# Kernel optimization log

Measured on AMD Instinct MI355X. Metric: run time of the kernel, lower is better.

## Reference

```python
import jax, jax.numpy as jnp
import numpy as np

EPS = 1e-06
NUM_HEADS = 16
THETA = 10000.0


def rope_tables(grid_size, head_dim):
    # matches VisionRotaryEmbeddingFast: 2D rope, table shape [grid^2, head_dim]
    half = head_dim // 2
    freqs = 1.0 / THETA ** (jnp.arange(0, half, 2, dtype=jnp.float32) / half)
    freqs = jnp.concatenate([freqs, freqs], axis=0)  # [half]
    t = jnp.arange(grid_size, dtype=jnp.float32)
    f = jnp.outer(t, freqs)  # [grid, half]
    fh = jnp.broadcast_to(f[:, None, :], (grid_size, grid_size, half))
    fw = jnp.broadcast_to(f[None, :, :], (grid_size, grid_size, half))
    full = jnp.concatenate([fh, fw], axis=-1).reshape(-1, head_dim)  # [N, head_dim]
    return jnp.cos(full), jnp.sin(full)


def rotate_half(x):
    n = x.shape[-1] // 2
    return jnp.concatenate((-x[..., n:], x[..., :n]), axis=-1)


def rms_norm(x, gamma):
    var = jnp.mean(x * x, axis=-1, keepdims=True)
    return x * jax.lax.rsqrt(var + EPS) * gamma


def setup_inputs() -> dict:
    key = jax.random.key(0)
    ks = jax.random.split(key, 5)
    B, N, C = 32, 1024, 1024
    return {
        "x": jax.random.normal(ks[0], (B, N, C), dtype=jnp.float32),
        "qkv_w": jax.random.normal(ks[1], (C, 3 * C), dtype=jnp.float32) * (C ** -0.5),
        "qkv_b": jnp.zeros((3 * C,), dtype=jnp.float32),
        "proj_w": jax.random.normal(ks[2], (C, C), dtype=jnp.float32) * (C ** -0.5),
        "proj_b": jnp.zeros((C,), dtype=jnp.float32),
        "q_gamma": jnp.ones((C // NUM_HEADS,), dtype=jnp.float32),
        "k_gamma": jnp.ones((C // NUM_HEADS,), dtype=jnp.float32),
    }


def reference(x, qkv_w, qkv_b, proj_w, proj_b, q_gamma, k_gamma):
    B, N, C = x.shape
    H = NUM_HEADS
    hd = C // H
    grid = int(np.sqrt(N))
    cos, sin = rope_tables(grid, hd)  # [N, hd] each
    cos = cos[None, :, None, :]  # broadcast over [B, N, H, hd]
    sin = sin[None, :, None, :]

    qkv = (x @ qkv_w + qkv_b).reshape(B, N, 3, H, hd)
    q, k, v = qkv[:, :, 0], qkv[:, :, 1], qkv[:, :, 2]  # [B, N, H, hd]

    q = rms_norm(q, q_gamma)
    k = rms_norm(k, k_gamma)
    q = q * cos + rotate_half(q) * sin
    k = k * cos + rotate_half(k) * sin

    out = jax.nn.dot_product_attention(q, k, v, is_causal=False)  # [B, N, H, hd]
    out = out.reshape(B, N, C)
    return out @ proj_w + proj_b
```

## Files before the change

kernel.cpp:

```cpp
#include <hip/hip_runtime.h>
#include <stdint.h>

typedef float f32x4 __attribute__((ext_vector_type(4)));
typedef short s16x8 __attribute__((ext_vector_type(8)));
typedef unsigned short u16;

__device__ __forceinline__ u16 f2bf(float f) {
  union { float f; uint32_t u; } c; c.f = f;
  uint32_t u = c.u;
  u = (u + 0x7fffu + ((u >> 16) & 1u)) >> 16;
  return (u16)u;
}

__device__ __forceinline__ u16 f2bf_fast(float f) {
  union { float f; uint32_t u; } c; c.f = f;
  return (u16)((c.u + 0x8000u) >> 16);
}

__device__ __forceinline__ void gload16(const void* g, void* lds) {
  __builtin_amdgcn_global_load_lds(
      (const __attribute__((address_space(1))) void*)g,
      (__attribute__((address_space(3))) void*)lds, 16, 0, 0);
}

__device__ __forceinline__ f32x4 mfma16(s16x8 a, s16x8 b, f32x4 c) {
  return __builtin_amdgcn_mfma_f32_16x16x32_bf16(a, b, c, 0, 0, 0);
}

__device__ __forceinline__ int swz(int row, int c8) {
  return row * 64 + ((c8 ^ (row & 7)) << 3);
}

__global__ void cvt_bf16(const float* __restrict__ in, u16* __restrict__ out, size_t n) {
  size_t i = ((size_t)blockIdx.x * blockDim.x + threadIdx.x) * 4;
  if (i < n) {
    float4 v = *(const float4*)&in[i];
    u16 o0 = f2bf(v.x), o1 = f2bf(v.y), o2 = f2bf(v.z), o3 = f2bf(v.w);
    uint2 packed;
    packed.x = (uint32_t)o0 | ((uint32_t)o1 << 16);
    packed.y = (uint32_t)o2 | ((uint32_t)o3 << 16);
    *(uint2*)&out[i] = packed;
  }
}

__global__ void transpose_cvt(const float* __restrict__ in, u16* __restrict__ out,
                              int rows, int cols) {
  __shared__ float tile[64][65];
  const int c0 = blockIdx.x * 64, r0 = blockIdx.y * 64;
  const int tr = threadIdx.x >> 6, tc = threadIdx.x & 63;
#pragma unroll
  for (int i = 0; i < 16; i++) {
    int r = i * 4 + tr;
    tile[r][tc] = in[(size_t)(r0 + r) * cols + c0 + tc];
  }
  __syncthreads();
#pragma unroll
  for (int i = 0; i < 16; i++) {
    int oc = i * 4 + tr;
    out[(size_t)(c0 + oc) * rows + r0 + tc] = f2bf(tile[tc][oc]);
  }
}

__global__ void rope_tables_kernel(float* __restrict__ cosT, float* __restrict__ sinT) {
  int n = blockIdx.x;
  int d = threadIdx.x;
  int ph = n >> 5, pw = n & 31;
  int pos = (d < 32) ? ph : pw;
  int fi = d & 15;
  float freq = powf(10000.f, -(float)fi / 16.f);
  float ang = (float)pos * freq;
  cosT[n * 64 + d] = cosf(ang);
  sinT[n * 64 + d] = sinf(ang);
}

__device__ __forceinline__ void gemm_mainloop_1024(
    const u16* __restrict__ Ag, const u16* __restrict__ Bg,
    u16* As, u16* Bs, f32x4 (&acc)[4][4])
{
  const int t = threadIdx.x;
  const int l = t & 63, w = t >> 6;
  const int wm = w >> 1, wn = w & 1;
  const int lrow = l & 15, lk8 = (l >> 4) * 8;
  const int row0 = t >> 2, cc = (t & 3) * 8;

  for (int kt = 0; kt < 1024; kt += 32) {
    gload16(Ag + (size_t)row0 * 1024 + kt + cc,        &As[w * 512]);
    gload16(Ag + (size_t)(row0 + 64) * 1024 + kt + cc, &As[2048 + w * 512]);
    gload16(Bg + (size_t)row0 * 1024 + kt + cc,        &Bs[w * 512]);
    gload16(Bg + (size_t)(row0 + 64) * 1024 + kt + cc, &Bs[2048 + w * 512]);
    asm volatile("s_waitcnt vmcnt(0)" ::: "memory");
    __syncthreads();

    s16x8 af[4], bfr[4];
#pragma unroll
    for (int mt = 0; mt < 4; mt++)
      af[mt] = *(const s16x8*)&As[(wm * 64 + mt * 16 + lrow) * 32 + lk8];
#pragma unroll
    for (int nt = 0; nt < 4; nt++)
      bfr[nt] = *(const s16x8*)&Bs[(wn * 64 + nt * 16 + lrow) * 32 + lk8];
#pragma unroll
    for (int mt = 0; mt < 4; mt++)
#pragma unroll
      for (int nt = 0; nt < 4; nt++)
        acc[mt][nt] = mfma16(af[mt], bfr[nt], acc[mt][nt]);
    __syncthreads();
  }
}

__global__ __launch_bounds__(256, 2) void gemm_qkv(
    const u16* __restrict__ A,
    const u16* __restrict__ Bt,
    const float* __restrict__ bias,
    const float* __restrict__ qgam, const float* __restrict__ kgam,
    const float* __restrict__ cosT, const float* __restrict__ sinT,
    u16* __restrict__ qb, u16* __restrict__ kb, u16* __restrict__ vb)
{
  __shared__ u16 As[4096], Bs[4096];
  const int bn = blockIdx.x, bm = blockIdx.y;

  const f32x4 fzero = {0.f, 0.f, 0.f, 0.f};
  f32x4 acc[4][4];
#pragma unroll
  for (int i = 0; i < 4; i++)
#pragma unroll
    for (int j = 0; j < 4; j++) acc[i][j] = fzero;

  gemm_mainloop_1024(A + (size_t)bm * 128 * 1024, Bt + (size_t)bn * 128 * 1024, As, Bs, acc);

  const int t = threadIdx.x, l = t & 63, w = t >> 6;
  const int wm = w >> 1, wn = w & 1, lrow = l & 15, lg = l >> 4;
  const int colb = bn * 128 + wn * 64;
  const int s = colb >> 10;
  const int h = (colb & 1023) >> 6;

  float biasv[4], g[4];
#pragma unroll
  for (int nt = 0; nt < 4; nt++) biasv[nt] = bias[colb + nt * 16 + lrow];
  const float* gamma = (s == 0) ? qgam : kgam;
#pragma unroll
  for (int nt = 0; nt < 4; nt++) g[nt] = gamma[nt * 16 + lrow];

  if (s < 2) {
    u16* dst = (s == 0) ? qb : kb;
    const float mul = (s == 0) ? 0.18033688011112042f : 1.0f;
#pragma unroll
    for (int mt = 0; mt < 4; mt++) {
#pragma unroll
      for (int r = 0; r < 4; r++) {
        const int rowg = bm * 128 + wm * 64 + mt * 16 + lg * 4 + r;
        const int b = rowg >> 10, np = rowg & 1023;
        float tmp[4]; float sq = 0.f;
#pragma unroll
        for (int nt = 0; nt < 4; nt++) {
          float v = acc[mt][nt][r] + biasv[nt];
          tmp[nt] = v; sq += v * v;
        }
#pragma unroll
        for (int off = 1; off < 16; off <<= 1) sq += __shfl_xor(sq, off);
        const float rstd = rsqrtf(sq * 0.015625f + 1e-6f);
#pragma unroll
        for (int nt = 0; nt < 4; nt++) tmp[nt] *= rstd * g[nt];
        const size_t base = (((size_t)(b * 16 + h)) * 1024 + np) * 64;
#pragma unroll
        for (int nt = 0; nt < 4; nt++) {
          const int d = nt * 16 + lrow;
          const float cv = cosT[np * 64 + d], sv = sinT[np * 64 + d];
          const float rh = (nt < 2) ? -tmp[nt + 2] : tmp[nt - 2];
          dst[base + d] = f2bf((tmp[nt] * cv + rh * sv) * mul);
        }
      }
    }
  } else {
#pragma unroll
    for (int mt = 0; mt < 4; mt++) {
#pragma unroll
      for (int r = 0; r < 4; r++) {
        const int rowg = bm * 128 + wm * 64 + mt * 16 + lg * 4 + r;
        const int b = rowg >> 10, np = rowg & 1023;
        const size_t hb = ((size_t)(b * 16 + h)) * 64;
#pragma unroll
        for (int nt = 0; nt < 4; nt++) {
          const int d = nt * 16 + lrow;
          vb[(hb + d) * 1024 + np] = f2bf(acc[mt][nt][r] + biasv[nt]);
        }
      }
    }
  }
}

__global__ __launch_bounds__(256, 3) void attn_kernel(
    const u16* __restrict__ qbuf, const u16* __restrict__ kbuf,
    const u16* __restrict__ vtbuf, u16* __restrict__ obuf)
{
  __shared__ u16 Qs[128 * 64];
  __shared__ u16 Ks[64 * 64];
  __shared__ u16 VTs[64 * 64];
  __shared__ u16 Ps[128 * 64];
  const int bx = blockIdx.x;
  const int bh = bx >> 3, qt = bx & 7;
  const int t = threadIdx.x, l = t & 63, w = t >> 6;
  const int lrow = l & 15, lg = l >> 4;

  const u16* qg  = qbuf  + (size_t)bh * 65536 + (size_t)qt * 8192;
  const u16* kg0 = kbuf  + (size_t)bh * 65536;
  const u16* vt0 = vtbuf + (size_t)bh * 65536;

  const int srow = l >> 3;
  const int sc8  = (l & 7) ^ (srow & 7);

#pragma unroll
  for (int i = 0; i < 4; i++) {
    const int r0 = (w + i * 4) * 8;
    gload16(qg + (size_t)(r0 + srow) * 64 + sc8 * 8, &Qs[r0 * 64]);
  }
#pragma unroll
  for (int i = 0; i < 2; i++) {
    const int r0 = (w + i * 4) * 8;
    gload16(kg0 + (size_t)(r0 + srow) * 64 + sc8 * 8, &Ks[r0 * 64]);
    gload16(vt0 + (size_t)(r0 + srow) * 1024 + sc8 * 8, &VTs[r0 * 64]);
  }
  asm volatile("s_waitcnt vmcnt(0)" ::: "memory");
  __syncthreads();

  s16x8 aq[2][2];
#pragma unroll
  for (int mt = 0; mt < 2; mt++)
#pragma unroll
    for (int kh = 0; kh < 2; kh++)
      aq[mt][kh] = *(const s16x8*)&Qs[swz(w * 32 + mt * 16 + lrow, kh * 4 + lg)];

  const f32x4 fzero = {0.f, 0.f, 0.f, 0.f};
  f32x4 o[2][4];
  float l_[2][4];
#pragma unroll
  for (int mt = 0; mt < 2; mt++) {
#pragma unroll
    for (int dt = 0; dt < 4; dt++) o[mt][dt] = fzero;
#pragma unroll
    for (int r = 0; r < 4; r++) l_[mt][r] = 0.f;
  }

  for (int kt = 0; kt < 16; kt++) {
    s16x8 bk[4][2];
#pragma unroll
    for (int nt = 0; nt < 4; nt++)
#pragma unroll
      for (int kh = 0; kh < 2; kh++)
        bk[nt][kh] = *(const s16x8*)&Ks[swz(nt * 16 + lrow, kh * 4 + lg)];

    f32x4 sf[2][4];
#pragma unroll
    for (int mt = 0; mt < 2; mt++)
#pragma unroll
      for (int nt = 0; nt < 4; nt++) {
        f32x4 z = fzero;
        z = mfma16(aq[mt][0], bk[nt][0], z);
        z = mfma16(aq[mt][1], bk[nt][1], z);
        sf[mt][nt] = z;
      }

#pragma unroll
    for (int mt = 0; mt < 2; mt++) {
      const int rowb = w * 32 + mt * 16 + lg * 4;
#pragma unroll
      for (int r = 0; r < 4; r++) {
        const int row = rowb + r;
        u16* prow = &Ps[row * 64 + (lrow & 7)];
        const int rm = row & 7;
        float acc_l = 0.f;
#pragma unroll
        for (int nt = 0; nt < 4; nt++) {
          float p = __builtin_amdgcn_exp2f(sf[mt][nt][r]);
          acc_l += p;
          prow[((nt * 2 + (lrow >> 3)) ^ rm) << 3] = f2bf_fast(p);
        }
        l_[mt][r] += acc_l;
      }
    }
    asm volatile("s_waitcnt lgkmcnt(0)" ::: "memory");

    s16x8 ap[2][2], bv[4][2];
#pragma unroll
    for (int mt = 0; mt < 2; mt++)
#pragma unroll
      for (int kh = 0; kh < 2; kh++)
        ap[mt][kh] = *(const s16x8*)&Ps[swz(w * 32 + mt * 16 + lrow, kh * 4 + lg)];
#pragma unroll
    for (int dt = 0; dt < 4; dt++)
#pragma unroll
      for (int kh = 0; kh < 2; kh++)
        bv[dt][kh] = *(const s16x8*)&VTs[swz(dt * 16 + lrow, kh * 4 + lg)];
#pragma unroll
    for (int mt = 0; mt < 2; mt++)
#pragma unroll
      for (int dt = 0; dt < 4; dt++) {
        o[mt][dt] = mfma16(ap[mt][0], bv[dt][0], o[mt][dt]);
        o[mt][dt] = mfma16(ap[mt][1], bv[dt][1], o[mt][dt]);
      }

    __syncthreads();
    if (kt < 15) {
      const int kb = (kt + 1) * 64;
#pragma unroll
      for (int i = 0; i < 2; i++) {
        const int r0 = (w + i * 4) * 8;
        gload16(kg0 + (size_t)(kb + r0 + srow) * 64 + sc8 * 8, &Ks[r0 * 64]);
        gload16(vt0 + (size_t)(r0 + srow) * 1024 + kb + sc8 * 8, &VTs[r0 * 64]);
      }
      asm volatile("s_waitcnt vmcnt(0)" ::: "memory");
      __syncthreads();
    }
  }

  const int b = bh >> 4, h = bh & 15;
#pragma unroll
  for (int mt = 0; mt < 2; mt++)
#pragma unroll
    for (int r = 0; r < 4; r++) {
      float lsum = l_[mt][r];
#pragma unroll
      for (int off = 1; off < 16; off <<= 1) lsum += __shfl_xor(lsum, off);
      const float inv = 1.0f / lsum;
      const int n = qt * 128 + w * 32 + mt * 16 + lg * 4 + r;
      const size_t base = (((size_t)b * 1024 + n) * 16 + h) * 64;
#pragma unroll
      for (int dt = 0; dt < 4; dt++)
        obuf[base + dt * 16 + lrow] = f2bf(o[mt][dt][r] * inv);
    }
}

__global__ __launch_bounds__(256, 2) void gemm_proj(
    const u16* __restrict__ A,
    const u16* __restrict__ Bt,
    const float* __restrict__ bias,
    float* __restrict__ out)
{
  __shared__ u16 As[4096], Bs[4096];
  const int bn = blockIdx.x, bm = blockIdx.y;

  const f32x4 fzero = {0.f, 0.f, 0.f, 0.f};
  f32x4 acc[4][4];
#pragma unroll
  for (int i = 0; i < 4; i++)
#pragma unroll
    for (int j = 0; j < 4; j++) acc[i][j] = fzero;

  gemm_mainloop_1024(A + (size_t)bm * 128 * 1024, Bt + (size_t)bn * 128 * 1024, As, Bs, acc);

  const int t = threadIdx.x, l = t & 63, w = t >> 6;
  const int wm = w >> 1, wn = w & 1, lrow = l & 15, lg = l >> 4;
  float biasv[4];
#pragma unroll
  for (int nt = 0; nt < 4; nt++) biasv[nt] = bias[bn * 128 + wn * 64 + nt * 16 + lrow];

#pragma unroll
  for (int mt = 0; mt < 4; mt++) {
#pragma unroll
    for (int r = 0; r < 4; r++) {
      const int rowg = bm * 128 + wm * 64 + mt * 16 + lg * 4 + r;
#pragma unroll
      for (int nt = 0; nt < 4; nt++) {
        const int col = bn * 128 + wn * 64 + nt * 16 + lrow;
        out[(size_t)rowg * 1024 + col] = acc[mt][nt][r] + biasv[nt];
      }
    }
  }
}

extern "C" void kernel_launch(void* const* d_in, const int* in_sizes, int n_in,
                              void* d_out, int out_size, void* d_ws, size_t ws_size,
                              hipStream_t stream) {
  const float* x      = (const float*)d_in[0];
  const float* qkv_w  = (const float*)d_in[1];
  const float* qkv_b  = (const float*)d_in[2];
  const float* proj_w = (const float*)d_in[3];
  const float* proj_b = (const float*)d_in[4];
  const float* q_gam  = (const float*)d_in[5];
  const float* k_gam  = (const float*)d_in[6];

  char* ws = (char*)d_ws;
  u16*   xb   = (u16*)(ws);
  u16*   qb   = (u16*)(ws + 67108864);
  u16*   kb   = (u16*)(ws + 134217728);
  u16*   vb   = (u16*)(ws + 201326592);
  u16*   wqT  = (u16*)(ws + 268435456);
  u16*   wpT  = (u16*)(ws + 274726912);
  float* cosT = (float*)(ws + 276824064);
  float* sinT = (float*)(ws + 277086208);
  u16*   attn = xb;

  cvt_bf16<<<32768, 256, 0, stream>>>(x, xb, (size_t)33554432);
  transpose_cvt<<<dim3(48, 16), 256, 0, stream>>>(qkv_w, wqT, 1024, 3072);
  transpose_cvt<<<dim3(16, 16), 256, 0, stream>>>(proj_w, wpT, 1024, 1024);
  rope_tables_kernel<<<1024, 64, 0, stream>>>(cosT, sinT);

  gemm_qkv<<<dim3(24, 256), 256, 0, stream>>>(xb, wqT, qkv_b, q_gam, k_gam,
                                              cosT, sinT, qb, kb, vb);
  attn_kernel<<<4096, 256, 0, stream>>>(qb, kb, vb, attn);
  gemm_proj<<<dim3(8, 256), 256, 0, stream>>>(attn, wpT, proj_b, (float*)d_out);
}
```

Measured before the change: 795.5 us.

## Rewrite GEMM mainloop as 256x256 double-buffered 8-wave pipeline with swizzled LDS

Replaces the simple 128x128, k=32, fully-synchronous GEMM mainloop used by the QKV and projection GEMMs. The new loop uses 256x256 tiles, 8 waves and k=64 steps, double-buffers LDS and interleaves global->LDS prefetch with MFMA phases using s_setprio and barriers. It also adds XOR-swizzled LDS addressing and a block-index remap for L2 locality. The aim is to hide global load latency and raise data reuse, at the cost of 128KB of LDS per block, more accumulator registers and fragile hand-coded vmcnt accounting.

```diff
diff --git a/kernel.cpp b/kernel.cpp
--- a/kernel.cpp
+++ b/kernel.cpp
@@ -73,41 +73,110 @@
   sinT[n * 64 + d] = sinf(ang);
 }
 
-__device__ __forceinline__ void gemm_mainloop_1024(
+
+#define PH_MID \
+  __builtin_amdgcn_sched_barrier(0); \
+  __builtin_amdgcn_s_barrier(); \
+  asm volatile("s_waitcnt lgkmcnt(0)" ::: "memory"); \
+  __builtin_amdgcn_sched_barrier(0); \
+  __builtin_amdgcn_s_setprio(1);
+
+#define PH_END \
+  __builtin_amdgcn_s_setprio(0); \
+  __builtin_amdgcn_sched_barrier(0); \
+  __builtin_amdgcn_s_barrier(); \
+  __builtin_amdgcn_sched_barrier(0);
+
+#define STAGE(ldsoff, g) do { \
+    gload16((g) + (size_t)(w8 + srow) * 1024 + sc8 * 8,       &lds[(ldsoff) + w8 * 64]); \
+    gload16((g) + (size_t)(w8 + srow + 64) * 1024 + sc8 * 8,  &lds[(ldsoff) + (w8 + 64) * 64]); \
+  } while (0)
+
+#define RD_A(dst, BUF, mh) \
+  _Pragma("unroll") \
+  for (int mi = 0; mi < 4; mi++) { \
+    dst[mi][0] = *(const s16x8*)&lds[(BUF) * 32768 + arow0 + ((mh) * 64 + mi * 16) * 64 + swz0]; \
+    dst[mi][1] = *(const s16x8*)&lds[(BUF) * 32768 + arow0 + ((mh) * 64 + mi * 16) * 64 + swz1]; \
+  }
+
+#define RD_B(dst, BUF, nh) \
+  _Pragma("unroll") \
+  for (int ni = 0; ni < 2; ni++) { \
+    dst[ni][0] = *(const s16x8*)&lds[(BUF) * 32768 + 16384 + brow0 + ((nh) * 32 + ni * 16) * 64 + swz0]; \
+    dst[ni][1] = *(const s16x8*)&lds[(BUF) * 32768 + 16384 + brow0 + ((nh) * 32 + ni * 16) * 64 + swz1]; \
+  }
+
+#define MFMA_QUAD(af, bfr, mh, nh) \
+  _Pragma("unroll") \
+  for (int mi = 0; mi < 4; mi++) \
+    _Pragma("unroll") \
+    for (int ni = 0; ni < 2; ni++) { \
+      acc[(mh) * 4 + mi][(nh) * 2 + ni] = mfma16(af[mi][0], bfr[ni][0], acc[(mh) * 4 + mi][(nh) * 2 + ni]); \
+      acc[(mh) * 4 + mi][(nh) * 2 + ni] = mfma16(af[mi][1], bfr[ni][1], acc[(mh) * 4 + mi][(nh) * 2 + ni]); \
+    }
+
+#define KTILE(BUF, KT, MODE) do { \
+    s16x8 a0f[4][2], a1f[4][2], b0f[2][2], b1f[2][2]; \
+     \
+    RD_A(a0f, BUF, 0); \
+    RD_B(b0f, BUF, 0); \
+    if ((MODE) < 2) STAGE((1 - (BUF)) * 32768, Ag + (size_t)((KT) + 1) * 64); \
+    PH_MID; MFMA_QUAD(a0f, b0f, 0, 0); PH_END; \
+     \
+    RD_B(b1f, BUF, 1); \
+    if ((MODE) < 2) STAGE((1 - (BUF)) * 32768 + 8192, Ag + (size_t)128 * 1024 + ((KT) + 1) * 64); \
+    PH_MID; MFMA_QUAD(a0f, b1f, 0, 1); PH_END; \
+     \
+    RD_A(a1f, BUF, 1); \
+    if ((MODE) == 0) STAGE((BUF) * 32768 + 16384, Bg + (size_t)((KT) + 2) * 64); \
+    PH_MID; MFMA_QUAD(a1f, b1f, 1, 1); PH_END; \
+     \
+    if ((MODE) == 0) STAGE((BUF) * 32768 + 16384 + 8192, Bg + (size_t)128 * 1024 + ((KT) + 2) * 64); \
+    PH_MID; MFMA_QUAD(a1f, b0f, 1, 0); \
+    __builtin_amdgcn_s_setprio(0); \
+    if ((MODE) == 0) asm volatile("s_waitcnt vmcnt(4)" ::: "memory"); \
+    if ((MODE) == 1) asm volatile("s_waitcnt vmcnt(0)" ::: "memory"); \
+    __builtin_amdgcn_sched_barrier(0); \
+    __builtin_amdgcn_s_barrier(); \
+    __builtin_amdgcn_sched_barrier(0); \
+  } while (0)
+
+__device__ __forceinline__ void gemm_mainloop_8ph(
     const u16* __restrict__ Ag, const u16* __restrict__ Bg,
-    u16* As, u16* Bs, f32x4 (&acc)[4][4])
+    u16* lds, f32x4 (&acc)[8][4])
 {
   const int t = threadIdx.x;
   const int l = t & 63, w = t >> 6;
-  const int wm = w >> 1, wn = w & 1;
-  const int lrow = l & 15, lk8 = (l >> 4) * 8;
-  const int row0 = t >> 2, cc = (t & 3) * 8;
-
-  for (int kt = 0; kt < 1024; kt += 32) {
-    gload16(Ag + (size_t)row0 * 1024 + kt + cc,        &As[w * 512]);
-    gload16(Ag + (size_t)(row0 + 64) * 1024 + kt + cc, &As[2048 + w * 512]);
-    gload16(Bg + (size_t)row0 * 1024 + kt + cc,        &Bs[w * 512]);
-    gload16(Bg + (size_t)(row0 + 64) * 1024 + kt + cc, &Bs[2048 + w * 512]);
-    asm volatile("s_waitcnt vmcnt(0)" ::: "memory");
-    __syncthreads();
-
-    s16x8 af[4], bfr[4];
-#pragma unroll
-    for (int mt = 0; mt < 4; mt++)
-      af[mt] = *(const s16x8*)&As[(wm * 64 + mt * 16 + lrow) * 32 + lk8];
-#pragma unroll
-    for (int nt = 0; nt < 4; nt++)
-      bfr[nt] = *(const s16x8*)&Bs[(wn * 64 + nt * 16 + lrow) * 32 + lk8];
-#pragma unroll
-    for (int mt = 0; mt < 4; mt++)
-#pragma unroll
-      for (int nt = 0; nt < 4; nt++)
-        acc[mt][nt] = mfma16(af[mt], bfr[nt], acc[mt][nt]);
-    __syncthreads();
-  }
-}
-
-__global__ __launch_bounds__(256, 2) void gemm_qkv(
+  const int wm = w & 1, wn = w >> 1;
+  const int lrow = l & 15, lg = l >> 4;
+  const int srow = l >> 3, sc8 = (l & 7) ^ srow;
+  const int w8 = w * 8;
+  const int swz0 = ((0 + lg) ^ (lrow & 7)) << 3;
+  const int swz1 = ((4 + lg) ^ (lrow & 7)) << 3;
+  const int arow0 = (wm * 128 + lrow) * 64;
+  const int brow0 = (wn * 64 + lrow) * 64;
+
+  STAGE(0,                 Ag);
+  STAGE(8192,              Ag + (size_t)128 * 1024);
+  STAGE(16384,             Bg);
+  STAGE(16384 + 8192,      Bg + (size_t)128 * 1024);
+  STAGE(32768 + 16384,          Bg + 64);
+  STAGE(32768 + 16384 + 8192,   Bg + (size_t)128 * 1024 + 64);
+  asm volatile("s_waitcnt vmcnt(4)" ::: "memory");
+  __builtin_amdgcn_sched_barrier(0);
+  __builtin_amdgcn_s_barrier();
+  __builtin_amdgcn_sched_barrier(0);
+
+#pragma unroll 1
+  for (int kt = 0; kt < 14; kt += 2) {
+    KTILE(0, kt, 0);
+    KTILE(1, kt + 1, 0);
+  }
+  KTILE(0, 14, 1);
+  KTILE(1, 15, 2);
+}
+
+__global__ __launch_bounds__(512, 2) void gemm_qkv(
     const u16* __restrict__ A,
     const u16* __restrict__ Bt,
     const float* __restrict__ bias,
@@ -115,21 +184,23 @@
     const float* __restrict__ cosT, const float* __restrict__ sinT,
     u16* __restrict__ qb, u16* __restrict__ kb, u16* __restrict__ vb)
 {
-  __shared__ u16 As[4096], Bs[4096];
-  const int bn = blockIdx.x, bm = blockIdx.y;
+  __shared__ u16 lds[65536];
+  const int bid = blockIdx.x;
+  const int sb = (bid & 7) * 192 + (bid >> 3);
+  const int bm = sb / 12, bn = sb % 12;
 
   const f32x4 fzero = {0.f, 0.f, 0.f, 0.f};
-  f32x4 acc[4][4];
-#pragma unroll
-  for (int i = 0; i < 4; i++)
+  f32x4 acc[8][4];
+#pragma unroll
+  for (int i = 0; i < 8; i++)
 #pragma unroll
     for (int j = 0; j < 4; j++) acc[i][j] = fzero;
 
-  gemm_mainloop_1024(A + (size_t)bm * 128 * 1024, Bt + (size_t)bn * 128 * 1024, As, Bs, acc);
+  gemm_mainloop_8ph(A + (size_t)bm * 256 * 1024, Bt + (size_t)bn * 256 * 1024, lds, acc);
 
   const int t = threadIdx.x, l = t & 63, w = t >> 6;
-  const int wm = w >> 1, wn = w & 1, lrow = l & 15, lg = l >> 4;
-  const int colb = bn * 128 + wn * 64;
+  const int wm = w & 1, wn = w >> 1, lrow = l & 15, lg = l >> 4;
+  const int colb = bn * 256 + wn * 64;
   const int s = colb >> 10;
   const int h = (colb & 1023) >> 6;
 
@@ -144,15 +215,15 @@
     u16* dst = (s == 0) ? qb : kb;
     const float mul = (s == 0) ? 0.18033688011112042f : 1.0f;
 #pragma unroll
-    for (int mt = 0; mt < 4; mt++) {
+    for (int mf = 0; mf < 8; mf++) {
 #pragma unroll
       for (int r = 0; r < 4; r++) {
-        const int rowg = bm * 128 + wm * 64 + mt * 16 + lg * 4 + r;
+        const int rowg = bm * 256 + wm * 128 + mf * 16 + lg * 4 + r;
         const int b = rowg >> 10, np = rowg & 1023;
         float tmp[4]; float sq = 0.f;
 #pragma unroll
         for (int nt = 0; nt < 4; nt++) {
-          float v = acc[mt][nt][r] + biasv[nt];
+          float v = acc[mf][nt][r] + biasv[nt];
           tmp[nt] = v; sq += v * v;
         }
 #pragma unroll
@@ -172,16 +243,16 @@
     }
   } else {
 #pragma unroll
-    for (int mt = 0; mt < 4; mt++) {
+    for (int mf = 0; mf < 8; mf++) {
 #pragma unroll
       for (int r = 0; r < 4; r++) {
-        const int rowg = bm * 128 + wm * 64 + mt * 16 + lg * 4 + r;
+        const int rowg = bm * 256 + wm * 128 + mf * 16 + lg * 4 + r;
         const int b = rowg >> 10, np = rowg & 1023;
         const size_t hb = ((size_t)(b * 16 + h)) * 64;
 #pragma unroll
         for (int nt = 0; nt < 4; nt++) {
           const int d = nt * 16 + lrow;
-          vb[(hb + d) * 1024 + np] = f2bf(acc[mt][nt][r] + biasv[nt]);
+          vb[(hb + d) * 1024 + np] = f2bf(acc[mf][nt][r] + biasv[nt]);
         }
       }
     }
@@ -329,39 +400,42 @@
     }
 }
 
-__global__ __launch_bounds__(256, 2) void gemm_proj(
+__global__ __launch_bounds__(512, 2) void gemm_proj(
     const u16* __restrict__ A,
     const u16* __restrict__ Bt,
     const float* __restrict__ bias,
     float* __restrict__ out)
 {
-  __shared__ u16 As[4096], Bs[4096];
-  const int bn = blockIdx.x, bm = blockIdx.y;
+  __shared__ u16 lds[65536];
+  const int bid = blockIdx.x;
+  const int sb = (bid & 7) * 64 + (bid >> 3);
+  const int bm = sb >> 2, bn = sb & 3;
 
   const f32x4 fzero = {0.f, 0.f, 0.f, 0.f};
-  f32x4 acc[4][4];
-#pragma unroll
-  for (int i = 0; i < 4; i++)
+  f32x4 acc[8][4];
+#pragma unroll
+  for (int i = 0; i < 8; i++)
 #pragma unroll
     for (int j = 0; j < 4; j++) acc[i][j] = fzero;
 
-  gemm_mainloop_1024(A + (size_t)bm * 128 * 1024, Bt + (size_t)bn * 128 * 1024, As, Bs, acc);
+  gemm_mainloop_8ph(A + (size_t)bm * 256 * 1024, Bt + (size_t)bn * 256 * 1024, lds, acc);
 
   const int t = threadIdx.x, l = t & 63, w = t >> 6;
-  const int wm = w >> 1, wn = w & 1, lrow = l & 15, lg = l >> 4;
+  const int wm = w & 1, wn = w >> 1, lrow = l & 15, lg = l >> 4;
+  const int colb = bn * 256 + wn * 64;
   float biasv[4];
 #pragma unroll
-  for (int nt = 0; nt < 4; nt++) biasv[nt] = bias[bn * 128 + wn * 64 + nt * 16 + lrow];
-
-#pragma unroll
-  for (int mt = 0; mt < 4; mt++) {
+  for (int nt = 0; nt < 4; nt++) biasv[nt] = bias[colb + nt * 16 + lrow];
+
+#pragma unroll
+  for (int mf = 0; mf < 8; mf++) {
 #pragma unroll
     for (int r = 0; r < 4; r++) {
-      const int rowg = bm * 128 + wm * 64 + mt * 16 + lg * 4 + r;
+      const int rowg = bm * 256 + wm * 128 + mf * 16 + lg * 4 + r;
 #pragma unroll
       for (int nt = 0; nt < 4; nt++) {
-        const int col = bn * 128 + wn * 64 + nt * 16 + lrow;
-        out[(size_t)rowg * 1024 + col] = acc[mt][nt][r] + biasv[nt];
+        const int col = colb + nt * 16 + lrow;
+        out[(size_t)rowg * 1024 + col] = acc[mf][nt][r] + biasv[nt];
       }
     }
   }
@@ -394,8 +468,8 @@
   transpose_cvt<<<dim3(16, 16), 256, 0, stream>>>(proj_w, wpT, 1024, 1024);
   rope_tables_kernel<<<1024, 64, 0, stream>>>(cosT, sinT);
 
-  gemm_qkv<<<dim3(24, 256), 256, 0, stream>>>(xb, wqT, qkv_b, q_gam, k_gam,
-                                              cosT, sinT, qb, kb, vb);
+  gemm_qkv<<<dim3(1536), dim3(512), 0, stream>>>(xb, wqT, qkv_b, q_gam, k_gam,
+                                                 cosT, sinT, qb, kb, vb);
   attn_kernel<<<4096, 256, 0, stream>>>(qb, kb, vb, attn);
-  gemm_proj<<<dim3(8, 256), 256, 0, stream>>>(attn, wpT, proj_b, (float*)d_out);
-}
+  gemm_proj<<<dim3(512), dim3(512), 0, stream>>>(attn, wpT, proj_b, (float*)d_out);
+}
```

Result: faster. 734.8 us (-7.6%).
